# Kernel tuning notes

Hardware: AMD Instinct MI355X
Metric: run time of the kernel (lower is better)

The kernel has to match this reference:

```python
import jax, jax.numpy as jnp
import numpy as np


def _nms_j(hm):
    """Vectorized equivalent of the numpy nms_j loop.

    In the original, disable[p] is set iff some 8-neighbor q has
    heatmap[q] >= heatmap[p] (all comparisons use the ORIGINAL values,
    so iteration order is irrelevant). Suppressed pixels are scaled by 0.6.
    """
    H, W = hm.shape
    p = jnp.pad(hm, 1, constant_values=-np.inf)
    shifts = [p[1 + dy:H + 1 + dy, 1 + dx:W + 1 + dx]
              for dy in (-1, 0, 1) for dx in (-1, 0, 1)
              if not (dy == 0 and dx == 0)]
    nmax = jnp.max(jnp.stack(shifts, axis=0), axis=0)  # max over 8 neighbors
    return jnp.where(nmax >= hm, 0.6 * hm, hm)


def _decode(hm, off):
    """post_jheatmap for one image: NMS, full descending sort, offset apply.

    Returns [H*W, 3] rows of (y, x, score) with sub-pixel offsets and +0.5.
    """
    H, W = hm.shape
    jmap = _nms_j(hm)
    flat = jmap.ravel()
    order = jnp.argsort(-flat)          # descending score order
    scores = flat[order]
    ys = order // W
    xs = order % W
    # offset[1] = y-offset, offset[0] = x-offset; gather at integer coords
    yo = off[1].ravel()[order]
    xo = off[0].ravel()[order]
    cy = ys.astype(jnp.float32) + yo + 0.5
    cx = xs.astype(jnp.float32) + xo + 0.5
    return jnp.stack([cy, cx, scores], axis=1)


def setup_inputs() -> dict:
    key = jax.random.key(0)
    k1, k2 = jax.random.split(key)
    B, H, W = 64, 512, 512
    heatmap = jax.random.uniform(k1, (B, H, W), dtype=jnp.float32)
    offset = jax.random.uniform(k2, (B, 2, H, W), dtype=jnp.float32) - 0.5
    return {"heatmap": heatmap, "offset": offset}


def reference(heatmap, offset):
    # [B, H*W, 3]
    return jax.vmap(_decode)(heatmap, offset)
```

## Files before the change

### kernel.cpp

```cpp
#include <hip/hip_runtime.h>
#include <stdint.h>

#define NIMG 64
#define H 512
#define W 512
#define NPIX (H * W)
#define LOGW 9
#define NC 256
#define BLK_ELEMS 4096
#define BLOCKS_PER_IMG (NPIX / BLK_ELEMS)
#define NPART (NIMG * BLOCKS_PER_IMG)
#define SEGCAP 2048

typedef unsigned int uint32;
typedef unsigned long long ull;

__device__ __forceinline__ float compute_jm(const float* __restrict__ base,
                                            int p, int y, int x) {
    float c = base[p];
    float nmax = -3.402823466e38f;
    bool ym = (y > 0), yp = (y < H - 1), xm = (x > 0), xp = (x < W - 1);
    if (ym) {
        const float* r = base + (p - W);
        if (xm) nmax = fmaxf(nmax, r[-1]);
        nmax = fmaxf(nmax, r[0]);
        if (xp) nmax = fmaxf(nmax, r[1]);
    }
    {
        const float* r = base + p;
        if (xm) nmax = fmaxf(nmax, r[-1]);
        if (xp) nmax = fmaxf(nmax, r[1]);
    }
    if (yp) {
        const float* r = base + (p + W);
        if (xm) nmax = fmaxf(nmax, r[-1]);
        nmax = fmaxf(nmax, r[0]);
        if (xp) nmax = fmaxf(nmax, r[1]);
    }
    return (nmax >= c) ? 0.6f * c : c;
}

__device__ __forceinline__ int bucket_of(float s) {
    int braw = (int)(s * 65536.0f);
    braw = braw > 65535 ? 65535 : braw;
    return 65535 - braw;
}

__global__ __launch_bounds__(256) void kA1_hist(const float* __restrict__ hm,
                                                uint32* __restrict__ counts) {
    __shared__ uint32 hist[NC];
    int blk = blockIdx.x;
    int img = blk >> 6;
    int lblk = blk & (BLOCKS_PER_IMG - 1);
    int t = threadIdx.x;
    hist[t] = 0;
    __syncthreads();
    const float* base = hm + (size_t)img * NPIX;
    int pbase = lblk * BLK_ELEMS;
#pragma unroll
    for (int r = 0; r < 16; ++r) {
        int p = pbase + r * 256 + t;
        int y = p >> LOGW, x = p & (W - 1);
        float jm = compute_jm(base, p, y, x);
        int cb = bucket_of(jm) >> 8;
        atomicAdd(&hist[cb], 1u);
    }
    __syncthreads();
    counts[((size_t)img * NC + t) * BLOCKS_PER_IMG + lblk] = hist[t];
}

__global__ __launch_bounds__(256) void kA2_scan(uint32* __restrict__ counts) {
    int img = blockIdx.x;
    int t = threadIdx.x;
    uint32* c = counts + (size_t)img * (NC * BLOCKS_PER_IMG);
    const int CH = (NC * BLOCKS_PER_IMG) / 256;
    int b0 = t * CH;
    uint32 s = 0;
    for (int i = 0; i < CH; ++i) s += c[b0 + i];
    __shared__ uint32 sums[256];
    sums[t] = s;
    __syncthreads();
    if (t == 0) {
        uint32 run = 0;
        for (int i = 0; i < 256; ++i) { uint32 v = sums[i]; sums[i] = run; run += v; }
    }
    __syncthreads();
    uint32 run = sums[t];
    for (int i = 0; i < CH; ++i) { uint32 v = c[b0 + i]; c[b0 + i] = run; run += v; }
}

__global__ __launch_bounds__(256) void kA3_part(const float* __restrict__ hm,
                                                const uint32* __restrict__ scan,
                                                ull* __restrict__ sorted) {
    __shared__ ull skeys[BLK_ELEMS];
    __shared__ uint32 hist[NC], gstart[NC], wofs[NC], sbase[NC], sc[NC];
    int blk = blockIdx.x;
    int img = blk >> 6;
    int lblk = blk & (BLOCKS_PER_IMG - 1);
    int t = threadIdx.x;
    hist[t] = 0;
    sbase[t] = scan[((size_t)img * NC + t) * BLOCKS_PER_IMG + lblk];
    __syncthreads();
    const float* base = hm + (size_t)img * NPIX;
    int pbase = lblk * BLK_ELEMS;
    ull keys[16];
    uint32 cbs[16];
#pragma unroll
    for (int r = 0; r < 16; ++r) {
        int p = pbase + r * 256 + t;
        int y = p >> LOGW, x = p & (W - 1);
        float jm = compute_jm(base, p, y, x);
        uint32 bits = __float_as_uint(jm);
        keys[r] = ((ull)(~bits) << 32) | (uint32)p;
        cbs[r] = (uint32)(bucket_of(jm) >> 8);
        atomicAdd(&hist[cbs[r]], 1u);
    }
    __syncthreads();
    uint32 v = hist[t];
    sc[t] = v;
    __syncthreads();
    for (int off = 1; off < 256; off <<= 1) {
        uint32 add = (t >= off) ? sc[t - off] : 0u;
        __syncthreads();
        sc[t] += add;
        __syncthreads();
    }
    gstart[t] = sc[t] - v;
    wofs[t] = sc[t] - v;
    __syncthreads();
#pragma unroll
    for (int r = 0; r < 16; ++r) {
        uint32 pos = atomicAdd(&wofs[cbs[r]], 1u);
        skeys[pos] = keys[r];
    }
    __syncthreads();
    ull* sout = sorted + (size_t)img * NPIX;
#pragma unroll
    for (int r = 0; r < 16; ++r) {
        int i = r * 256 + t;
        ull k = skeys[i];
        uint32 bits = ~(uint32)(k >> 32);
        float s = __uint_as_float(bits);
        int cb = bucket_of(s) >> 8;
        sout[sbase[cb] + (uint32)i - gstart[cb]] = k;
    }
}

__global__ __launch_bounds__(256) void kB_finalize(const ull* __restrict__ sorted,
                                                   const uint32* __restrict__ scan,
                                                   const float* __restrict__ offset,
                                                   float* __restrict__ out) {
    int img = blockIdx.x >> 8;
    int cb = blockIdx.x & (NC - 1);
    int t = threadIdx.x;
    const uint32* sc_img = scan + (size_t)img * (NC * BLOCKS_PER_IMG);
    uint32 cstart = sc_img[cb * BLOCKS_PER_IMG];
    uint32 cend = (cb < NC - 1) ? sc_img[(cb + 1) * BLOCKS_PER_IMG] : (uint32)NPIX;
    int len = (int)(cend - cstart);
    const ull* sin = sorted + (size_t)img * NPIX + cstart;
    const size_t obase2 = (size_t)img * 2 * NPIX;
    float* oseg = out + ((size_t)img * NPIX + cstart) * 3;

    if (len <= 0) return;

    if (len > SEGCAP) {
        for (int i = t; i < len; i += 256) {
            ull k = sin[i];
            int rank = 0;
            for (int q = 0; q < len; ++q) rank += (sin[q] < k) ? 1 : 0;
            uint32 bits = ~(uint32)(k >> 32);
            float s = __uint_as_float(bits);
            uint32 p0 = (uint32)k;
            int yy = (int)(p0 >> LOGW), xx = (int)(p0 & (W - 1));
            float yo = offset[obase2 + NPIX + p0];
            float xo = offset[obase2 + p0];
            oseg[(size_t)rank * 3 + 0] = (float)yy + yo + 0.5f;
            oseg[(size_t)rank * 3 + 1] = (float)xx + xo + 0.5f;
            oseg[(size_t)rank * 3 + 2] = s;
        }
        return;
    }

    __shared__ ull u0[SEGCAP * 3 / 2];
    __shared__ ull bufB[SEGCAP];
    __shared__ uint32 fhist[256], fscan[256], fcnt[256];
    ull* bufA = u0;
    float* rows = (float*)u0;

    for (int i = t; i < len; i += 256) bufA[i] = sin[i];
    fhist[t] = 0;
    __syncthreads();
    for (int i = t; i < len; i += 256) {
        ull k = bufA[i];
        float s = __uint_as_float(~(uint32)(k >> 32));
        int f = bucket_of(s) & 255;
        atomicAdd(&fhist[f], 1u);
    }
    __syncthreads();
    uint32 v = fhist[t];
    fscan[t] = v;
    __syncthreads();
    for (int off = 1; off < 256; off <<= 1) {
        uint32 add = (t >= off) ? fscan[t - off] : 0u;
        __syncthreads();
        fscan[t] += add;
        __syncthreads();
    }
    uint32 excl = fscan[t] - v;
    __syncthreads();
    fscan[t] = excl;
    fcnt[t] = excl;
    __syncthreads();
    for (int i = t; i < len; i += 256) {
        ull k = bufA[i];
        float s = __uint_as_float(~(uint32)(k >> 32));
        int f = bucket_of(s) & 255;
        uint32 pos = atomicAdd(&fcnt[f], 1u);
        bufB[pos] = k;
    }
    __syncthreads();
    for (int i = t; i < len; i += 256) {
        ull k = bufB[i];
        uint32 bits = ~(uint32)(k >> 32);
        float s = __uint_as_float(bits);
        int f = bucket_of(s) & 255;
        uint32 gs = fscan[f];
        uint32 ge = gs + fhist[f];
        int rank = 0;
        for (uint32 q = gs; q < ge; ++q) rank += (bufB[q] < k) ? 1 : 0;
        uint32 pos = gs + (uint32)rank;
        uint32 p0 = (uint32)k;
        int yy = (int)(p0 >> LOGW), xx = (int)(p0 & (W - 1));
        float yo = offset[obase2 + NPIX + p0];
        float xo = offset[obase2 + p0];
        rows[pos * 3 + 0] = (float)yy + yo + 0.5f;
        rows[pos * 3 + 1] = (float)xx + xo + 0.5f;
        rows[pos * 3 + 2] = s;
    }
    __syncthreads();
    int n3 = len * 3;
    for (int i = t; i < n3; i += 256) oseg[i] = rows[i];
}

extern "C" void kernel_launch(void* const* d_in, const int* in_sizes, int n_in,
                              void* d_out, int out_size, void* d_ws, size_t ws_size,
                              hipStream_t stream) {
    const float* hm = (const float*)d_in[0];
    const float* offset = (const float*)d_in[1];
    float* out = (float*)d_out;

    const size_t counts_elems = (size_t)NIMG * NC * BLOCKS_PER_IMG;
    uint32* counts = (uint32*)d_ws;
    ull* sorted = (ull*)((char*)d_ws + counts_elems * sizeof(uint32));

    hipMemsetAsync(counts, 0, counts_elems * sizeof(uint32), stream);

    kA1_hist<<<NPART, 256, 0, stream>>>(hm, counts);
    kA2_scan<<<NIMG, 256, 0, stream>>>(counts);
    kA3_part<<<NPART, 256, 0, stream>>>(hm, counts, sorted);
    kB_finalize<<<NIMG * NC, 256, 0, stream>>>(sorted, counts, offset, out);
}
```

Measured before the change: 841.5 us.

## Keep finalize keys in registers, alias LDS buffers, and interleave block-to-image mapping

```diff
diff --git a/kernel.cpp b/kernel.cpp
--- a/kernel.cpp
+++ b/kernel.cpp
@@ -150,8 +150,10 @@
                                                    const uint32* __restrict__ scan,
                                                    const float* __restrict__ offset,
                                                    float* __restrict__ out) {
-    int img = blockIdx.x >> 8;
-    int cb = blockIdx.x & (NC - 1);
+    int bid = blockIdx.x;
+    int g = bid >> 3;
+    int img = (bid & 7) + 8 * (g >> 8);
+    int cb = g & (NC - 1);
     int t = threadIdx.x;
     const uint32* sc_img = scan + (size_t)img * (NC * BLOCKS_PER_IMG);
     uint32 cstart = sc_img[cb * BLOCKS_PER_IMG];
@@ -171,30 +173,36 @@
             uint32 bits = ~(uint32)(k >> 32);
             float s = __uint_as_float(bits);
             uint32 p0 = (uint32)k;
-            int yy = (int)(p0 >> LOGW), xx = (int)(p0 & (W - 1));
             float yo = offset[obase2 + NPIX + p0];
             float xo = offset[obase2 + p0];
-            oseg[(size_t)rank * 3 + 0] = (float)yy + yo + 0.5f;
-            oseg[(size_t)rank * 3 + 1] = (float)xx + xo + 0.5f;
+            oseg[(size_t)rank * 3 + 0] = (float)(p0 >> LOGW) + yo + 0.5f;
+            oseg[(size_t)rank * 3 + 1] = (float)(p0 & (W - 1)) + xo + 0.5f;
             oseg[(size_t)rank * 3 + 2] = s;
         }
         return;
     }
 
-    __shared__ ull u0[SEGCAP * 3 / 2];
-    __shared__ ull bufB[SEGCAP];
+    __shared__ float rows[SEGCAP * 3];
+    ull* bufB = (ull*)rows;
     __shared__ uint32 fhist[256], fscan[256], fcnt[256];
-    ull* bufA = u0;
-    float* rows = (float*)u0;
-
-    for (int i = t; i < len; i += 256) bufA[i] = sin[i];
+
+    ull myk[8];
+    int myf[8];
+    uint32 mypos[8];
+
     fhist[t] = 0;
     __syncthreads();
-    for (int i = t; i < len; i += 256) {
-        ull k = bufA[i];
-        float s = __uint_as_float(~(uint32)(k >> 32));
-        int f = bucket_of(s) & 255;
-        atomicAdd(&fhist[f], 1u);
+#pragma unroll
+    for (int j = 0; j < 8; ++j) {
+        int i = t + j * 256;
+        if (i < len) {
+            ull k = sin[i];
+            myk[j] = k;
+            float s = __uint_as_float(~(uint32)(k >> 32));
+            int f = bucket_of(s) & 255;
+            myf[j] = f;
+            atomicAdd(&fhist[f], 1u);
+        }
     }
     __syncthreads();
     uint32 v = fhist[t];
@@ -211,31 +219,43 @@
     fscan[t] = excl;
     fcnt[t] = excl;
     __syncthreads();
-    for (int i = t; i < len; i += 256) {
-        ull k = bufA[i];
-        float s = __uint_as_float(~(uint32)(k >> 32));
-        int f = bucket_of(s) & 255;
-        uint32 pos = atomicAdd(&fcnt[f], 1u);
-        bufB[pos] = k;
-    }
-    __syncthreads();
-    for (int i = t; i < len; i += 256) {
-        ull k = bufB[i];
-        uint32 bits = ~(uint32)(k >> 32);
-        float s = __uint_as_float(bits);
-        int f = bucket_of(s) & 255;
-        uint32 gs = fscan[f];
-        uint32 ge = gs + fhist[f];
-        int rank = 0;
-        for (uint32 q = gs; q < ge; ++q) rank += (bufB[q] < k) ? 1 : 0;
-        uint32 pos = gs + (uint32)rank;
-        uint32 p0 = (uint32)k;
-        int yy = (int)(p0 >> LOGW), xx = (int)(p0 & (W - 1));
-        float yo = offset[obase2 + NPIX + p0];
-        float xo = offset[obase2 + p0];
-        rows[pos * 3 + 0] = (float)yy + yo + 0.5f;
-        rows[pos * 3 + 1] = (float)xx + xo + 0.5f;
-        rows[pos * 3 + 2] = s;
+#pragma unroll
+    for (int j = 0; j < 8; ++j) {
+        int i = t + j * 256;
+        if (i < len) {
+            uint32 pos = atomicAdd(&fcnt[myf[j]], 1u);
+            bufB[pos] = myk[j];
+        }
+    }
+    __syncthreads();
+#pragma unroll
+    for (int j = 0; j < 8; ++j) {
+        int i = t + j * 256;
+        if (i < len) {
+            ull k = myk[j];
+            int f = myf[j];
+            uint32 gs = fscan[f];
+            uint32 ge = gs + fhist[f];
+            int rank = 0;
+            for (uint32 q = gs; q < ge; ++q) rank += (bufB[q] < k) ? 1 : 0;
+            mypos[j] = gs + (uint32)rank;
+        }
+    }
+    __syncthreads();
+#pragma unroll
+    for (int j = 0; j < 8; ++j) {
+        int i = t + j * 256;
+        if (i < len) {
+            ull k = myk[j];
+            uint32 p0 = (uint32)k;
+            float s = __uint_as_float(~(uint32)(k >> 32));
+            float yo = offset[obase2 + NPIX + p0];
+            float xo = offset[obase2 + p0];
+            uint32 pos = mypos[j];
+            rows[pos * 3 + 0] = (float)(p0 >> LOGW) + yo + 0.5f;
+            rows[pos * 3 + 1] = (float)(p0 & (W - 1)) + xo + 0.5f;
+            rows[pos * 3 + 2] = s;
+        }
     }
     __syncthreads();
     int n3 = len * 3;
```

Result: faster. 744.4 us (-11.5%).
